# Kernel tuning notes

Measured on AMD Instinct MI355X. Metric: run time of the kernel, lower is better.

The kernel has to match this reference:

```python
import jax, jax.numpy as jnp
import numpy as np

B, OBS, L, D, BINS, HID = 4096, 128, 4, 8, 16, 512
S = L * D  # max_seq_len = 32; qchunk_size = S, single Q chunk


def _lin(k, i, o, s):
    kw, kb = jax.random.split(k)
    return jax.random.normal(kw, (i, o), jnp.float32) * s, jnp.zeros((o,), jnp.float32)


def setup_inputs() -> dict:
    key = jax.random.key(0)
    ks = jax.random.split(key, 12)
    inp = {
        "obs": jax.random.normal(ks[0], (B, OBS), jnp.float32),
        "category": jax.random.randint(ks[1], (B, L, D), 0, BINS, jnp.int32),
    }
    # v_network: obs_dim -> 512 -> 512 -> 512 -> 1 (tanh hidden)
    dims_v = [OBS, HID, HID, HID, 1]
    for i in range(4):
        w, b = _lin(ks[2 + i], dims_v[i], dims_v[i + 1], 0.05)
        inp[f"v_w{i}"], inp[f"v_b{i}"] = w, b
    # q_network: (obs_dim+actor_dim) -> 512 -> 512 -> 512 -> bins*S
    dims_q = [OBS + D, HID, HID, HID, BINS * S]
    for i in range(4):
        w, b = _lin(ks[6 + i], dims_q[i], dims_q[i + 1], 0.05)
        inp[f"q_w{i}"], inp[f"q_b{i}"] = w, b
    return inp


def _mlp(x, ws, bs):
    for w, b in zip(ws[:-1], bs[:-1]):
        x = jnp.tanh(x @ w + b)
    return x @ ws[-1] + bs[-1]


def _actions_from_category(category):
    # zoom_in per (level, dim): width_l = 2/bins^(l+1); low accumulates cat*width.
    cat = category.astype(jnp.float32)  # (B, L, D)
    widths = 2.0 / (jnp.float32(BINS) ** jnp.arange(1, L + 1, dtype=jnp.float32))  # (L,)
    cum_low = jnp.cumsum(cat * widths[None, :, None], axis=1)  # (B, L, D)
    mids = -1.0 + cum_low + 0.5 * widths[None, :, None]  # midpoint after each level
    # mids_full[:, j, d] = midpoint of dim d after j zoom-in updates (j=0 -> 0.0)
    mids_full = jnp.concatenate(
        [jnp.zeros((category.shape[0], 1, D), jnp.float32), mids], axis=1)  # (B, L+1, D)
    # at sequence step k (input to Q), dim d' has had U[k,d'] updates
    k = jnp.arange(S)
    U = k[:, None] // D + (jnp.arange(D)[None, :] < (k[:, None] % D)).astype(jnp.int32)  # (S, D)
    dgrid = jnp.broadcast_to(jnp.arange(D)[None, :], (S, D))
    return mids_full[:, U, dgrid]  # (B, S, D)


def reference(obs, category,
              v_w0, v_b0, v_w1, v_b1, v_w2, v_b2, v_w3, v_b3,
              q_w0, q_b0, q_w1, q_b1, q_w2, q_b2, q_w3, q_b3):
    vw = [v_w0, v_w1, v_w2, v_w3]; vb = [v_b0, v_b1, v_b2, v_b3]
    qw = [q_w0, q_w1, q_w2, q_w3]; qb = [q_b0, q_b1, q_b2, q_b3]
    b = obs.shape[0]
    actions = _actions_from_category(category)  # (B, S, D)
    obs_rep = jnp.broadcast_to(obs[:, None, :], (b, S, OBS))
    x = jnp.concatenate([obs_rep, actions], axis=-1)  # (B, S, OBS+D)
    adv = _mlp(x, qw, qb)  # (B, S, S*BINS)
    adv = adv.reshape(b, S, S, BINS)
    s_idx = jnp.arange(S)
    adv = adv[:, s_idx, s_idx, :]  # diagonal gather -> (B, S, BINS)
    adv = adv.reshape(b, L, D, BINS)
    value = _mlp(obs, vw, vb)  # (B, 1)
    nbias = jnp.zeros((b, L, D, 1), jnp.float32)  # use_nbias=False
    return value, adv, nbias
```

## Files before the change

### kernel.cpp

```cpp
#include <hip/hip_runtime.h>
#include <hip/hip_bf16.h>

#define B_SZ   4096
#define OBS_N  128
#define HID    512
#define TANH_K 2.885390081777927f


typedef __bf16 bf16x8_t __attribute__((ext_vector_type(8)));
typedef float  f32x4_t  __attribute__((ext_vector_type(4)));

__device__ inline float fast_tanh(float x) {
    float e = __builtin_amdgcn_exp2f(x * TANH_K);
    return fmaf(-2.f, __builtin_amdgcn_rcpf(e + 1.f), 1.f);
}

__device__ inline float tanh_u(float u) {
    float e = __builtin_amdgcn_exp2f(u);
    return fmaf(-2.f, __builtin_amdgcn_rcpf(e + 1.f), 1.f);
}

__device__ inline void gld_lds16(const void* g, void* l) {
    __builtin_amdgcn_global_load_lds(
        (const __attribute__((address_space(1))) void*)g,
        (__attribute__((address_space(3))) void*)l, 16, 0, 0);
}

__device__ inline int hs_off(int row, int col) {
    int c = col >> 3;
    int phys = (c & ~7) | ((c ^ (row & 7)) & 7);
    return row * 512 + phys * 8 + (col & 7);
}

__global__ __launch_bounds__(256) void prep_kernel(
    const float* __restrict__ obs, const int* __restrict__ category,
    const float* __restrict__ qw0, const float* __restrict__ qb0,
    const float* __restrict__ qw1, const float* __restrict__ qw2,
    const float* __restrict__ qw3,
    const float* __restrict__ vw0, const float* __restrict__ vb0,
    const float* __restrict__ vw1, const float* __restrict__ vw2,
    __hip_bfloat16* __restrict__ obs_bf,
    __hip_bfloat16* __restrict__ w0t, __hip_bfloat16* __restrict__ w1t,
    __hip_bfloat16* __restrict__ w2t, __hip_bfloat16* __restrict__ w3t,
    __hip_bfloat16* __restrict__ vw0t, __hip_bfloat16* __restrict__ vw1t,
    __hip_bfloat16* __restrict__ vw2t,
    __hip_bfloat16* __restrict__ w0aug, __hip_bfloat16* __restrict__ vw0aug,
    __hip_bfloat16* __restrict__ acts_bf, float* __restrict__ nbias)
{
    const int bid = blockIdx.x, tid = threadIdx.x;
    if (bid < 2048) {
        int i = bid * 256 + tid;
        obs_bf[i] = __float2bfloat16(obs[i]);
    } else if (bid < 2560) {
        const float* src = (bid < 2304) ? qw0 : vw0;
        __hip_bfloat16* dst = (bid < 2304) ? w0t : vw0t;
        int idx = ((bid - 2048) & 255) * 256 + tid;
        int n = idx >> 7, k = idx & 127;
        dst[idx] = __float2bfloat16(src[k * 512 + n]);
    } else if (bid < 7680) {
        int job = (bid - 2560) >> 10;
        const float* srcs[5] = {qw1, qw2, qw3, vw1, vw2};
        __hip_bfloat16* dsts[5] = {w1t, w2t, w3t, vw1t, vw2t};
        int idx = ((bid - 2560) & 1023) * 256 + tid;
        int e    = idx & 7;
        int lane = (idx >> 3) & 63;
        int kc   = (idx >> 9) & 15;
        int tile = idx >> 13;
        int k = kc * 32 + (lane >> 4) * 8 + e;
        int n = tile * 16 + (lane & 15);
        dsts[job][idx] = __float2bfloat16(srcs[job][k * 512 + n]);
    } else if (bid < 11776) {
        int t = (bid - 7680) * 256 + tid;
        int d = t & 7;
        int r = t >> 3;
        int b = r & 4095, s = r >> 12;
        int U = (s >> 3) + ((d < (s & 7)) ? 1 : 0);
        float a = 0.f;
        if (U > 0) {
            float w = 0.125f, cum = 0.f;
            for (int j = 0; j < U; ++j) {
                cum += (float)category[b * 32 + j * 8 + d] * w;
                if (j == U - 1) a = -1.f + cum + 0.5f * w;
                w *= 0.0625f;
            }
        }
        acts_bf[t] = __float2bfloat16(a);
    } else if (bid < 11904) {
        int sub = bid - 11776;
        bool isv = sub >= 64;
        int idx = (sub & 63) * 256 + tid;
        int e    = idx & 7;
        int lane = (idx >> 3) & 63;
        int tile = idx >> 9;
        int k = (lane >> 4) * 8 + e;
        int n = tile * 16 + (lane & 15);
        float v = 0.f;
        if (!isv) {
            if (k < 8) v = qw0[(128 + k) * 512 + n];
            else if (k == 8) v = qb0[n];
            w0aug[idx] = __float2bfloat16(v);
        } else {
            if (k == 8) v = vb0[n];
            vw0aug[idx] = __float2bfloat16(v);
        }
    } else {
        int i = (bid - 11904) * 256 + tid;
        nbias[i] = 0.f;
    }
}

__global__ __launch_bounds__(256) void gemm_dual(
    const __hip_bfloat16* __restrict__ A0, const __hip_bfloat16* __restrict__ B0,
    const float* __restrict__ bias0, void* __restrict__ C0, int K0, int epi0, int nb0,
    const __hip_bfloat16* __restrict__ A1, const __hip_bfloat16* __restrict__ B1,
    const float* __restrict__ bias1, void* __restrict__ C1, int K1, int epi1)
{
    __shared__ __hip_bfloat16 As[128 * 32];
    __shared__ __hip_bfloat16 Bs[128 * 32];

    const __hip_bfloat16 *A, *Bt;
    const float* bias;
    void* Cout;
    int K, epi, tb;
    if ((int)blockIdx.x < nb0) {
        A = A0; Bt = B0; bias = bias0; Cout = C0; K = K0; epi = epi0; tb = blockIdx.x;
    } else {
        A = A1; Bt = B1; bias = bias1; Cout = C1; K = K1; epi = epi1; tb = blockIdx.x - nb0;
    }
    const long m0 = (long)(tb >> 2) * 128;
    const int  n0 = (tb & 3) * 128;

    const int tid  = threadIdx.x;
    const int wave = tid >> 6, lane = tid & 63;
    const int quad = lane >> 4, t = lane & 15;
    const int wr = wave >> 1, wc = wave & 1;

    f32x4_t acc[4][4] = {};

    const int lrow  = lane >> 2;
    const int lkoff = (((lane & 3) + (lane >> 3)) & 3) * 8;

    const __hip_bfloat16* Ag0 = A  + (m0 + wave * 32 +      lrow) * (long)K + lkoff;
    const __hip_bfloat16* Ag1 = A  + (m0 + wave * 32 + 16 + lrow) * (long)K + lkoff;
    const __hip_bfloat16* Bg0 = Bt + (long)(n0 + wave * 32 +      lrow) * K + lkoff;
    const __hip_bfloat16* Bg1 = Bt + (long)(n0 + wave * 32 + 16 + lrow) * K + lkoff;
    __hip_bfloat16* AsB0 = &As[(wave * 32) * 32];
    __hip_bfloat16* AsB1 = &As[(wave * 32 + 16) * 32];
    __hip_bfloat16* BsB0 = &Bs[(wave * 32) * 32];
    __hip_bfloat16* BsB1 = &Bs[(wave * 32 + 16) * 32];

    const int slot = ((quad - (t >> 1)) & 3) * 8;

    for (int k0 = 0; k0 < K; k0 += 32) {
        gld_lds16(Ag0 + k0, AsB0);
        gld_lds16(Ag1 + k0, AsB1);
        gld_lds16(Bg0 + k0, BsB0);
        gld_lds16(Bg1 + k0, BsB1);
        __syncthreads();
        bf16x8_t af[4], bfr[4];
        #pragma unroll
        for (int i = 0; i < 4; ++i)
            af[i] = *(const bf16x8_t*)&As[(wr * 64 + i * 16 + t) * 32 + slot];
        #pragma unroll
        for (int j = 0; j < 4; ++j)
            bfr[j] = *(const bf16x8_t*)&Bs[(wc * 64 + j * 16 + t) * 32 + slot];
        #pragma unroll
        for (int i = 0; i < 4; ++i)
            #pragma unroll
            for (int j = 0; j < 4; ++j)
                acc[i][j] = __builtin_amdgcn_mfma_f32_16x16x32_bf16(af[i], bfr[j], acc[i][j], 0, 0, 0);
        __syncthreads();
    }

    #pragma unroll
    for (int i = 0; i < 4; ++i) {
        const long rbase = m0 + wr * 64 + i * 16 + quad * 4;
        #pragma unroll
        for (int j = 0; j < 4; ++j) {
            const int col = n0 + wc * 64 + j * 16 + t;
            #pragma unroll
            for (int r = 0; r < 4; ++r) {
                float v = acc[i][j][r];
                if (epi == 1) {
                    v = fast_tanh(v + bias[col]);
                    ((__hip_bfloat16*)Cout)[(rbase + r) * 512 + col] = __float2bfloat16(v);
                } else if (epi == 2) {
                    ((__hip_bfloat16*)Cout)[(rbase + r) * 512 + col] = __float2bfloat16(v);
                } else if (epi == 3) {
                    const long m = rbase + r;
                    const int brow = (int)(m & 63);
                    const long idx =
                        ((((m >> 6) * 8 + (col >> 6)) * 16 + (brow >> 4) * 4 + ((col >> 4) & 3)) * 256)
                        + ((col >> 2) & 3) * 64 + (brow & 15) * 4 + (col & 3);
                    ((float*)Cout)[idx] = v;
                } else {
                    ((float*)Cout)[(rbase + r) * 512 + col] = v;
                }
            }
        }
    }
}

__device__ inline void epi_store(
    __hip_bfloat16* hs, f32x4_t acc[4][4], const float* bias,
    int n0w, int quad, int t)
{
    #pragma unroll
    for (int j = 0; j < 4; ++j) {
        const int oc0 = n0w + j * 16 + quad * 4;
        float4 blK = {0.f, 0.f, 0.f, 0.f};
        if (bias) {
            float4 bl = *(const float4*)&bias[oc0];
            blK.x = bl.x * TANH_K; blK.y = bl.y * TANH_K;
            blK.z = bl.z * TANH_K; blK.w = bl.w * TANH_K;
        }
        const int cbase = oc0 >> 3;
        const int sub = (quad & 1) * 4;
        #pragma unroll
        for (int rt = 0; rt < 4; ++rt) {
            const int row = rt * 16 + t;
            union { __hip_bfloat16 b[4]; uint2 v; } o;
            o.b[0] = __float2bfloat16(tanh_u(fmaf(acc[rt][j][0], TANH_K, blK.x)));
            o.b[1] = __float2bfloat16(tanh_u(fmaf(acc[rt][j][1], TANH_K, blK.y)));
            o.b[2] = __float2bfloat16(tanh_u(fmaf(acc[rt][j][2], TANH_K, blK.z)));
            o.b[3] = __float2bfloat16(tanh_u(fmaf(acc[rt][j][3], TANH_K, blK.w)));
            const int phys = (cbase & ~7) | ((cbase ^ (row & 7)) & 7);
            *(uint2*)&hs[row * 512 + phys * 8 + sub] = o.v;
        }
    }
}

__device__ inline void mfma_layer(
    __hip_bfloat16* hs, const __hip_bfloat16* __restrict__ Wt,
    const float* __restrict__ bias, int w, int lane)
{
    const int quad = lane >> 4, t = lane & 15;
    const int n0w = w * 64;
    const __hip_bfloat16* Wl = Wt + ((size_t)(w * 4) * 16 * 64 + lane) * 8;
    const int pe = (quad ^ (t & 7)) & 7;
    int aOff0[4], aOff1[4];
    #pragma unroll
    for (int rt = 0; rt < 4; ++rt) {
        aOff0[rt] = (rt * 16 + t) * 512 + pe * 8;
        aOff1[rt] = (rt * 16 + t) * 512 + (pe ^ 4) * 8;
    }
    f32x4_t acc[4][4] = {};
    bf16x8_t wc[4], wn[4], ac[4];
    #pragma unroll
    for (int j = 0; j < 4; ++j)
        wc[j] = *(const bf16x8_t*)(Wl + (size_t)(j * 16) * 512);

    #pragma unroll 2
    for (int kc = 0; kc < 16; ++kc) {
        const int kb = (kc >> 1) * 64;
        #pragma unroll
        for (int rt = 0; rt < 4; ++rt)
            ac[rt] = *(const bf16x8_t*)&hs[((kc & 1) ? aOff1[rt] : aOff0[rt]) + kb];
        if (kc < 15) {
            #pragma unroll
            for (int j = 0; j < 4; ++j)
                wn[j] = *(const bf16x8_t*)(Wl + (size_t)(j * 16 + kc + 1) * 512);
        }
        #pragma unroll
        for (int j = 0; j < 4; ++j)
            #pragma unroll
            for (int rt = 0; rt < 4; ++rt)
                acc[rt][j] = __builtin_amdgcn_mfma_f32_16x16x32_bf16(wc[j], ac[rt], acc[rt][j], 0, 0, 0);
        #pragma unroll
        for (int j = 0; j < 4; ++j) wc[j] = wn[j];
    }
    __syncthreads();
    epi_store(hs, acc, bias, n0w, quad, t);
    __syncthreads();
}

__global__ __launch_bounds__(512, 4) void fused_kernel(
    const float* __restrict__ p,
    const float* __restrict__ pv,
    const __hip_bfloat16* __restrict__ acts_bf,
    const __hip_bfloat16* __restrict__ w0aug,
    const __hip_bfloat16* __restrict__ vw0aug,
    const __hip_bfloat16* __restrict__ w1t, const float* __restrict__ qb1,
    const __hip_bfloat16* __restrict__ w2t, const float* __restrict__ qb2,
    const __hip_bfloat16* __restrict__ w3t, const float* __restrict__ qb3,
    float* __restrict__ advout,
    const __hip_bfloat16* __restrict__ vw1t, const float* __restrict__ vb1,
    const __hip_bfloat16* __restrict__ vw2t, const float* __restrict__ vb2,
    const float* __restrict__ vw3, const float* __restrict__ vb3,
    float* __restrict__ vout)
{
    __shared__ __hip_bfloat16 hs[64 * 512];
    const int bid = blockIdx.x;
    const int tid = threadIdx.x;
    const int w = tid >> 6, lane = tid & 63;
    const int quad = lane >> 4, t = lane & 15;
    const bool is_q = bid < 2048;
    const int s  = is_q ? (bid >> 6) : 0;
    const int mb = is_q ? (bid & 63) : (bid - 2048);
    const int n0w = w * 64;

    {
        const float* Pt = (is_q ? p : pv) + (((size_t)mb * 8 + w) * 16) * 256 + lane * 4;
        const __hip_bfloat16* W0 = is_q ? w0aug : vw0aug;
        f32x4_t acc[4][4];
        #pragma unroll
        for (int rt = 0; rt < 4; ++rt)
            #pragma unroll
            for (int j = 0; j < 4; ++j)
                acc[rt][j] = *(const f32x4_t*)(Pt + (rt * 4 + j) * 256);
        bf16x8_t bfrag[4];
        #pragma unroll
        for (int rt = 0; rt < 4; ++rt) {
            union { bf16x8_t vec; unsigned short u[8]; } bu;
            #pragma unroll
            for (int i = 0; i < 8; ++i) bu.u[i] = 0;
            if (quad == 1) bu.u[0] = 0x3F80;
            if (is_q && quad == 0) {
                const long r = (long)s * 4096 + mb * 64 + rt * 16 + t;
                bu.vec = *(const bf16x8_t*)&acts_bf[r * 8];
            }
            bfrag[rt] = bu.vec;
        }
        bf16x8_t wq[4];
        #pragma unroll
        for (int j = 0; j < 4; ++j)
            wq[j] = *(const bf16x8_t*)(W0 + ((size_t)(w * 4 + j) * 64 + lane) * 8);
        #pragma unroll
        for (int j = 0; j < 4; ++j)
            #pragma unroll
            for (int rt = 0; rt < 4; ++rt)
                acc[rt][j] = __builtin_amdgcn_mfma_f32_16x16x32_bf16(wq[j], bfrag[rt], acc[rt][j], 0, 0, 0);
        epi_store(hs, acc, nullptr, n0w, quad, t);
    }
    __syncthreads();

    mfma_layer(hs, is_q ? w1t : vw1t, is_q ? qb1 : vb1, w, lane);
    mfma_layer(hs, is_q ? w2t : vw2t, is_q ? qb2 : vb2, w, lane);

    if (is_q) {
        f32x4_t acc = {};
        if (w < 4) {
            const __hip_bfloat16* W3l = w3t + ((size_t)s * 16 * 64 + (size_t)lane) * 8;
            const int pe = (quad ^ (t & 7)) & 7;
            const int o0 = (w * 16 + t) * 512 + pe * 8;
            const int o1 = (w * 16 + t) * 512 + (pe ^ 4) * 8;
            #pragma unroll 4
            for (int kc = 0; kc < 16; ++kc) {
                bf16x8_t a = *(const bf16x8_t*)&hs[((kc & 1) ? o1 : o0) + (kc >> 1) * 64];
                bf16x8_t bq = *(const bf16x8_t*)(W3l + (size_t)kc * 512);
                acc = __builtin_amdgcn_mfma_f32_16x16x32_bf16(a, bq, acc, 0, 0, 0);
            }
        }
        __syncthreads();
        float* hsf = (float*)hs;
        if (w < 4) {
            const float bias3 = qb3[s * 16 + t];
            #pragma unroll
            for (int rr = 0; rr < 4; ++rr)
                hsf[(w * 16 + quad * 4 + rr) * 16 + t] = acc[rr] + bias3;
        }
        __syncthreads();
        const int row = tid >> 3, cp = tid & 7;
        float2 v2 = *(const float2*)&hsf[row * 16 + cp * 2];
        *(float2*)&advout[(size_t)(mb * 64 + row) * 512 + s * 16 + cp * 2] = v2;
    } else {
        const int row = tid >> 3, seg = tid & 7;
        float sum = 0.f;
        for (int k = seg * 64; k < seg * 64 + 64; ++k)
            sum += __bfloat162float(hs[hs_off(row, k)]) * vw3[k];
        sum += __shfl_xor(sum, 1);
        sum += __shfl_xor(sum, 2);
        sum += __shfl_xor(sum, 4);
        if (seg == 0) vout[mb * 64 + row] = sum + vb3[0];
    }
}

extern "C" void kernel_launch(void* const* d_in, const int* in_sizes, int n_in,
                              void* d_out, int out_size, void* d_ws, size_t ws_size,
                              hipStream_t stream) {
    const float* obs      = (const float*)d_in[0];
    const int*   category = (const int*)d_in[1];
    const float* v_w0 = (const float*)d_in[2];
    const float* v_b0 = (const float*)d_in[3];
    const float* v_w1 = (const float*)d_in[4];
    const float* v_b1 = (const float*)d_in[5];
    const float* v_w2 = (const float*)d_in[6];
    const float* v_b2 = (const float*)d_in[7];
    const float* v_w3 = (const float*)d_in[8];
    const float* v_b3 = (const float*)d_in[9];
    const float* q_w0 = (const float*)d_in[10];
    const float* q_b0 = (const float*)d_in[11];
    const float* q_w1 = (const float*)d_in[12];
    const float* q_b1 = (const float*)d_in[13];
    const float* q_w2 = (const float*)d_in[14];
    const float* q_b2 = (const float*)d_in[15];
    const float* q_w3 = (const float*)d_in[16];
    const float* q_b3 = (const float*)d_in[17];

    char* ws = (char*)d_ws;
    __hip_bfloat16* obs_bf = (__hip_bfloat16*)(ws + 0);
    __hip_bfloat16* w0t    = (__hip_bfloat16*)(ws + 1048576);
    __hip_bfloat16* vw0t   = (__hip_bfloat16*)(ws + 1179648);
    __hip_bfloat16* w1t    = (__hip_bfloat16*)(ws + 1310720);
    __hip_bfloat16* w2t    = (__hip_bfloat16*)(ws + 1835008);
    __hip_bfloat16* w3t    = (__hip_bfloat16*)(ws + 2359296);
    __hip_bfloat16* vw1t   = (__hip_bfloat16*)(ws + 2883584);
    __hip_bfloat16* vw2t   = (__hip_bfloat16*)(ws + 3407872);
    __hip_bfloat16* w0aug  = (__hip_bfloat16*)(ws + 3932160);
    __hip_bfloat16* vw0aug = (__hip_bfloat16*)(ws + 3964928);
    __hip_bfloat16* acts_bf= (__hip_bfloat16*)(ws + 3997696);
    float*          p      = (float*)         (ws + 6094848);
    float*          pv     = (float*)         (ws + 14483456);

    float* out       = (float*)d_out;
    float* out_value = out;
    float* out_adv   = out + 4096;
    float* out_nbias = out + 4096 + (size_t)B_SZ * 512;

    prep_kernel<<<12416, 256, 0, stream>>>(
        obs, category, q_w0, q_b0, q_w1, q_w2, q_w3, v_w0, v_b0, v_w1, v_w2,
        obs_bf, w0t, w1t, w2t, w3t, vw0t, vw1t, vw2t, w0aug, vw0aug,
        acts_bf, out_nbias);

    gemm_dual<<<256, 256, 0, stream>>>(
        obs_bf, w0t, nullptr, p, 128, 3, 128,
        obs_bf, vw0t, nullptr, pv, 128, 3);

    fused_kernel<<<2112, 512, 0, stream>>>(
        p, pv, acts_bf, w0aug, vw0aug, w1t, q_b1, w2t, q_b2, w3t, q_b3, out_adv,
        vw1t, v_b1, vw2t, v_b2, v_w3, v_b3, out_value);
}
```

Baseline: 271.9 us.

## Tile weight transposes through LDS and prefetch next-layer weights across layers

The prep kernel now transposes and converts weights to bf16 in 16-column tiles. It reads coalesced float4 rows into shared memory and writes 16-byte vectors, replacing the strided per-element gathers. The grid shrinks from 12416 to 7008 blocks. In the fused kernel, each layer's first weight fragments are loaded before the previous layer's epilogue and barrier, and the last-layer loop is software-pipelined, to hide global load latency. The cost is more live registers, which could pressure occupancy under the launch bounds.

```diff
diff --git a/kernel.cpp b/kernel.cpp
--- a/kernel.cpp
+++ b/kernel.cpp
@@ -47,30 +47,65 @@
     __hip_bfloat16* __restrict__ w0aug, __hip_bfloat16* __restrict__ vw0aug,
     __hip_bfloat16* __restrict__ acts_bf, float* __restrict__ nbias)
 {
+    __shared__ __hip_bfloat16 ts[512 * 16];
     const int bid = blockIdx.x, tid = threadIdx.x;
     if (bid < 2048) {
         int i = bid * 256 + tid;
         obs_bf[i] = __float2bfloat16(obs[i]);
-    } else if (bid < 2560) {
-        const float* src = (bid < 2304) ? qw0 : vw0;
-        __hip_bfloat16* dst = (bid < 2304) ? w0t : vw0t;
-        int idx = ((bid - 2048) & 255) * 256 + tid;
-        int n = idx >> 7, k = idx & 127;
-        dst[idx] = __float2bfloat16(src[k * 512 + n]);
-    } else if (bid < 7680) {
-        int job = (bid - 2560) >> 10;
+    } else if (bid < 2112) {
+        int b2 = bid - 2048;
+        bool isv = b2 >= 32;
+        const float* src = isv ? vw0 : qw0;
+        __hip_bfloat16* dst = isv ? vw0t : w0t;
+        int tilen = (b2 & 31) * 16;
+        #pragma unroll
+        for (int pss = 0; pss < 2; ++pss) {
+            int k = pss * 64 + (tid >> 2);
+            int nl = (tid & 3) * 4;
+            float4 v = *(const float4*)&src[(size_t)k * 512 + tilen + nl];
+            ts[k * 16 + nl + 0] = __float2bfloat16(v.x);
+            ts[k * 16 + nl + 1] = __float2bfloat16(v.y);
+            ts[k * 16 + nl + 2] = __float2bfloat16(v.z);
+            ts[k * 16 + nl + 3] = __float2bfloat16(v.w);
+        }
+        __syncthreads();
+        int n_loc = tid >> 4, kc8 = (tid & 15) * 8;
+        union { bf16x8_t vec; __hip_bfloat16 e[8]; } o;
+        #pragma unroll
+        for (int e = 0; e < 8; ++e) o.e[e] = ts[(kc8 + e) * 16 + n_loc];
+        *(bf16x8_t*)&dst[(size_t)(tilen + n_loc) * 128 + kc8] = o.vec;
+    } else if (bid < 2272) {
+        int b2 = bid - 2112;
+        int job = b2 >> 5;
+        int tile = b2 & 31;
         const float* srcs[5] = {qw1, qw2, qw3, vw1, vw2};
         __hip_bfloat16* dsts[5] = {w1t, w2t, w3t, vw1t, vw2t};
-        int idx = ((bid - 2560) & 1023) * 256 + tid;
-        int e    = idx & 7;
-        int lane = (idx >> 3) & 63;
-        int kc   = (idx >> 9) & 15;
-        int tile = idx >> 13;
-        int k = kc * 32 + (lane >> 4) * 8 + e;
-        int n = tile * 16 + (lane & 15);
-        dsts[job][idx] = __float2bfloat16(srcs[job][k * 512 + n]);
-    } else if (bid < 11776) {
-        int t = (bid - 7680) * 256 + tid;
+        const float* src = srcs[job];
+        __hip_bfloat16* dst = dsts[job];
+        #pragma unroll
+        for (int pss = 0; pss < 8; ++pss) {
+            int k = pss * 64 + (tid >> 2);
+            int nl = (tid & 3) * 4;
+            float4 v = *(const float4*)&src[(size_t)k * 512 + tile * 16 + nl];
+            ts[k * 16 + nl + 0] = __float2bfloat16(v.x);
+            ts[k * 16 + nl + 1] = __float2bfloat16(v.y);
+            ts[k * 16 + nl + 2] = __float2bfloat16(v.z);
+            ts[k * 16 + nl + 3] = __float2bfloat16(v.w);
+        }
+        __syncthreads();
+        #pragma unroll
+        for (int q = 0; q < 4; ++q) {
+            int kc = q * 4 + (tid >> 6);
+            int lane = tid & 63;
+            int kbase = kc * 32 + (lane >> 4) * 8;
+            int n = lane & 15;
+            union { bf16x8_t vec; __hip_bfloat16 e[8]; } o;
+            #pragma unroll
+            for (int e = 0; e < 8; ++e) o.e[e] = ts[(kbase + e) * 16 + n];
+            *(bf16x8_t*)&dst[((size_t)(tile * 16 + kc) * 64 + lane) * 8] = o.vec;
+        }
+    } else if (bid < 6368) {
+        int t = (bid - 2272) * 256 + tid;
         int d = t & 7;
         int r = t >> 3;
         int b = r & 4095, s = r >> 12;
@@ -85,8 +120,8 @@
             }
         }
         acts_bf[t] = __float2bfloat16(a);
-    } else if (bid < 11904) {
-        int sub = bid - 11776;
+    } else if (bid < 6496) {
+        int sub = bid - 6368;
         bool isv = sub >= 64;
         int idx = (sub & 63) * 256 + tid;
         int e    = idx & 7;
@@ -104,7 +139,7 @@
             vw0aug[idx] = __float2bfloat16(v);
         }
     } else {
-        int i = (bid - 11904) * 256 + tid;
+        int i = (bid - 6496) * 256 + tid;
         nbias[i] = 0.f;
     }
 }
@@ -231,12 +266,13 @@
 }
 
 __device__ inline void mfma_layer(
-    __hip_bfloat16* hs, const __hip_bfloat16* __restrict__ Wt,
-    const float* __restrict__ bias, int w, int lane)
+    __hip_bfloat16* hs, const __hip_bfloat16* __restrict__ Wl,
+    const float* __restrict__ bias, int w, int lane,
+    bf16x8_t wc0[4], const __hip_bfloat16* __restrict__ Wlnext,
+    bf16x8_t wpre[4])
 {
     const int quad = lane >> 4, t = lane & 15;
     const int n0w = w * 64;
-    const __hip_bfloat16* Wl = Wt + ((size_t)(w * 4) * 16 * 64 + lane) * 8;
     const int pe = (quad ^ (t & 7)) & 7;
     int aOff0[4], aOff1[4];
     #pragma unroll
@@ -247,8 +283,7 @@
     f32x4_t acc[4][4] = {};
     bf16x8_t wc[4], wn[4], ac[4];
     #pragma unroll
-    for (int j = 0; j < 4; ++j)
-        wc[j] = *(const bf16x8_t*)(Wl + (size_t)(j * 16) * 512);
+    for (int j = 0; j < 4; ++j) wc[j] = wc0[j];
 
     #pragma unroll 2
     for (int kc = 0; kc < 16; ++kc) {
@@ -268,6 +303,11 @@
                 acc[rt][j] = __builtin_amdgcn_mfma_f32_16x16x32_bf16(wc[j], ac[rt], acc[rt][j], 0, 0, 0);
         #pragma unroll
         for (int j = 0; j < 4; ++j) wc[j] = wn[j];
+    }
+    if (Wlnext) {
+        #pragma unroll
+        for (int j = 0; j < 4; ++j)
+            wpre[j] = *(const bf16x8_t*)(Wlnext + (size_t)(j * 16) * 512);
     }
     __syncthreads();
     epi_store(hs, acc, bias, n0w, quad, t);
@@ -299,6 +339,13 @@
     const int mb = is_q ? (bid & 63) : (bid - 2048);
     const int n0w = w * 64;
 
+    const __hip_bfloat16* W1l = (is_q ? w1t : vw1t) + ((size_t)(w * 4) * 16 * 64 + lane) * 8;
+    const __hip_bfloat16* W2l = (is_q ? w2t : vw2t) + ((size_t)(w * 4) * 16 * 64 + lane) * 8;
+    const __hip_bfloat16* W3l = (is_q && w < 4)
+        ? w3t + ((size_t)s * 16 * 64 + (size_t)lane) * 8 : nullptr;
+
+    bf16x8_t wc1[4], wc2[4], wc3[4];
+
     {
         const float* Pt = (is_q ? p : pv) + (((size_t)mb * 8 + w) * 16) * 256 + lane * 4;
         const __hip_bfloat16* W0 = is_q ? w0aug : vw0aug;
@@ -330,25 +377,29 @@
             #pragma unroll
             for (int rt = 0; rt < 4; ++rt)
                 acc[rt][j] = __builtin_amdgcn_mfma_f32_16x16x32_bf16(wq[j], bfrag[rt], acc[rt][j], 0, 0, 0);
+        #pragma unroll
+        for (int j = 0; j < 4; ++j)
+            wc1[j] = *(const bf16x8_t*)(W1l + (size_t)(j * 16) * 512);
         epi_store(hs, acc, nullptr, n0w, quad, t);
     }
     __syncthreads();
 
-    mfma_layer(hs, is_q ? w1t : vw1t, is_q ? qb1 : vb1, w, lane);
-    mfma_layer(hs, is_q ? w2t : vw2t, is_q ? qb2 : vb2, w, lane);
+    mfma_layer(hs, W1l, is_q ? qb1 : vb1, w, lane, wc1, W2l, wc2);
+    mfma_layer(hs, W2l, is_q ? qb2 : vb2, w, lane, wc2, W3l, wc3);
 
     if (is_q) {
         f32x4_t acc = {};
         if (w < 4) {
-            const __hip_bfloat16* W3l = w3t + ((size_t)s * 16 * 64 + (size_t)lane) * 8;
             const int pe = (quad ^ (t & 7)) & 7;
             const int o0 = (w * 16 + t) * 512 + pe * 8;
             const int o1 = (w * 16 + t) * 512 + (pe ^ 4) * 8;
+            bf16x8_t b_cur = wc3[0], b_next;
             #pragma unroll 4
             for (int kc = 0; kc < 16; ++kc) {
                 bf16x8_t a = *(const bf16x8_t*)&hs[((kc & 1) ? o1 : o0) + (kc >> 1) * 64];
-                bf16x8_t bq = *(const bf16x8_t*)(W3l + (size_t)kc * 512);
-                acc = __builtin_amdgcn_mfma_f32_16x16x32_bf16(a, bq, acc, 0, 0, 0);
+                if (kc < 15) b_next = *(const bf16x8_t*)(W3l + (size_t)(kc + 1) * 512);
+                acc = __builtin_amdgcn_mfma_f32_16x16x32_bf16(a, b_cur, acc, 0, 0, 0);
+                b_cur = b_next;
             }
         }
         __syncthreads();
@@ -417,7 +468,7 @@
     float* out_adv   = out + 4096;
     float* out_nbias = out + 4096 + (size_t)B_SZ * 512;
 
-    prep_kernel<<<12416, 256, 0, stream>>>(
+    prep_kernel<<<7008, 256, 0, stream>>>(
         obs, category, q_w0, q_b0, q_w1, q_w2, q_w3, v_w0, v_b0, v_w1, v_w2,
         obs_bf, w0t, w1t, w2t, w3t, vw0t, vw1t, vw2t, w0aug, vw0aug,
         acts_bf, out_nbias);
```

After: 273.0 us. No clear change (+0.4%).
